# Kernel optimization log

Hardware: AMD Instinct MI355X
Metric: run time of the kernel (lower is better)

## Reference

```python
import jax, jax.numpy as jnp
import numpy as np

E = 1024
H = 16
HD = 64
LN_EPS = 1e-5


def _layernorm(x, g, b):
    mu = jnp.mean(x, axis=-1, keepdims=True)
    var = jnp.mean((x - mu) ** 2, axis=-1, keepdims=True)
    return (x - mu) * jax.lax.rsqrt(var + LN_EPS) * g + b


def _positional(L):
    # PositionalEncoding: stepper = 1/10000^(arange(0,E,2)/E); cat(sin, cos) -> [L, E]
    stepper = 1.0 / (10000.0 ** (jnp.arange(0, E, 2, dtype=jnp.float32) / E))
    args = jnp.arange(L, dtype=jnp.float32)[:, None] * stepper[None, :]  # [L, E/2]
    return jnp.concatenate([jnp.sin(args), jnp.cos(args)], axis=1)  # [L, E]


def setup_inputs() -> dict:
    key = jax.random.key(0)
    ks = jax.random.split(key, 8)
    s = 1.0 / np.sqrt(E)
    return {
        "sequences": jax.random.normal(ks[0], (4, 2048, E), dtype=jnp.float32),
        "W_q": jax.random.normal(ks[1], (E, E), dtype=jnp.float32) * s,
        "W_k": jax.random.normal(ks[2], (E, E), dtype=jnp.float32) * s,
        "W_v": jax.random.normal(ks[3], (E, E), dtype=jnp.float32) * s,
        "W_o": jax.random.normal(ks[4], (E, E), dtype=jnp.float32) * s,
        "ln1_g": jnp.ones((E,), jnp.float32),
        "ln1_b": jnp.zeros((E,), jnp.float32),
        "lin_W": jax.random.normal(ks[5], (E, E), dtype=jnp.float32) * s,  # torch Linear weight [out,in]
        "lin_b": jnp.zeros((E,), jnp.float32),
        "ln2_g": jnp.ones((E,), jnp.float32),
        "ln2_b": jnp.zeros((E,), jnp.float32),
    }


def reference(sequences, W_q, W_k, W_v, W_o, ln1_g, ln1_b, lin_W, lin_b, ln2_g, ln2_b):
    B, L, _ = sequences.shape
    x = sequences + _positional(L)[None]  # add positional embeddings
    # projections (no bias)
    q = (x @ W_q).reshape(B, L, H, HD).transpose(0, 2, 1, 3)  # [B,H,L,hd]
    k = (x @ W_k).reshape(B, L, H, HD).transpose(0, 2, 1, 3)
    v = (x @ W_v).reshape(B, L, H, HD).transpose(0, 2, 1, 3)
    # linear (softmax-free) attention: (Q K^T / sqrt(hd)) V
    scores = jnp.einsum("bhqd,bhkd->bhqk", q, k) / jnp.sqrt(jnp.float32(HD))
    ctx = jnp.einsum("bhqk,bhkd->bhqd", scores, v)
    ctx = ctx.transpose(0, 2, 1, 3).reshape(B, L, E)
    attn_out = ctx @ W_o
    h = _layernorm(x + attn_out, ln1_g, ln1_b)
    ff = jax.nn.relu(h @ lin_W.T + lin_b)
    return _layernorm(ff + h, ln2_g, ln2_b)
```

## Files before the change

kernel.cpp:

```cpp
#include <hip/hip_runtime.h>
#include <cstdint>

typedef unsigned short u16;
typedef __bf16 bf16x8 __attribute__((ext_vector_type(8)));
typedef float f32x4 __attribute__((ext_vector_type(4)));

__device__ __forceinline__ u16 f2bf(float f) {
    unsigned u = __float_as_uint(f);
    u += 0x7fffu + ((u >> 16) & 1u);
    return (u16)(u >> 16);
}
__device__ __forceinline__ float bf2f(u16 h) {
    return __uint_as_float(((unsigned)h) << 16);
}

__device__ __forceinline__ void lds16(const void* g, void* l) {
    __builtin_amdgcn_global_load_lds(
        (const __attribute__((address_space(1))) void*)g,
        (__attribute__((address_space(3))) void*)l, 16, 0, 0);
}

__global__ __launch_bounds__(256) void prep_x(const float* __restrict__ seq,
                                              float* __restrict__ x,
                                              u16* __restrict__ xb) {
    size_t i = (size_t)blockIdx.x * 256 + threadIdx.x;
    int e4 = (int)(i & 255) * 4;
    int l  = (int)((i >> 8) & 2047);
    float4 s = ((const float4*)seq)[i];
    float v[4] = {s.x, s.y, s.z, s.w};
    const float c = -13.287712379549449f / 512.0f;
#pragma unroll
    for (int j = 0; j < 4; j++) {
        int e  = e4 + j;
        int ii = e & 511;
        float st  = exp2f(c * (float)ii);
        float arg = (float)l * st;
        v[j] += (e < 512) ? sinf(arg) : cosf(arg);
    }
    float4 o; o.x = v[0]; o.y = v[1]; o.z = v[2]; o.w = v[3];
    ((float4*)x)[i] = o;
    ushort4 ob; ob.x = f2bf(v[0]); ob.y = f2bf(v[1]); ob.z = f2bf(v[2]); ob.w = f2bf(v[3]);
    ((ushort4*)xb)[i] = ob;
}

__global__ void prep_w(const float* __restrict__ wq, const float* __restrict__ wk,
                       const float* __restrict__ wv, const float* __restrict__ wo,
                       const float* __restrict__ wl, u16* __restrict__ wt) {
    int mat = blockIdx.z;
    const float* src = (mat == 0) ? wq : (mat == 1) ? wk : (mat == 2) ? wv : (mat == 3) ? wo : wl;
    u16* dst = wt + (size_t)mat * 1024 * 1024;
    int tx = threadIdx.x, ty = threadIdx.y;
    if (mat == 4) {
        int col = blockIdx.x * 32 + tx, row0 = blockIdx.y * 32;
#pragma unroll
        for (int j = 0; j < 32; j += 8)
            dst[(size_t)(row0 + ty + j) * 1024 + col] = f2bf(src[(size_t)(row0 + ty + j) * 1024 + col]);
    } else {
        __shared__ float tile[32][33];
        int col = blockIdx.x * 32 + tx, row0 = blockIdx.y * 32;
#pragma unroll
        for (int j = 0; j < 32; j += 8)
            tile[ty + j][tx] = src[(size_t)(row0 + ty + j) * 1024 + col];
        __syncthreads();
        int col2 = blockIdx.y * 32 + tx, row20 = blockIdx.x * 32;
#pragma unroll
        for (int j = 0; j < 32; j += 8)
            dst[(size_t)(row20 + ty + j) * 1024 + col2] = f2bf(tile[tx][ty + j]);
    }
}

template <int EPI>
__global__ __launch_bounds__(512) void gemm8p(const u16* __restrict__ A,
                                              const u16* __restrict__ Bt,
                                              void* __restrict__ Cv,
                                              const float* __restrict__ bias,
                                              int N, int K, int lda, size_t bstride) {
    __shared__ __align__(16) u16 lds[49152];
    const int t = threadIdx.x;
    const int ntn = N >> 8;
    const int nwg = gridDim.x;
    int bid = (int)blockIdx.x;
    bid = (bid & 7) * (nwg >> 3) + (bid >> 3);
    const int tm = bid / ntn, tn = bid - tm * ntn;
    const size_t m0 = (size_t)tm << 7, n0 = (size_t)tn << 8;
    const int w = t >> 6, lane = t & 63;
    const int wr = w >> 2, wc = w & 3;
    const u16* Bt_e = Bt + (bstride ? (m0 >> 11) * bstride : 0);

    const int r0 = t >> 3;
    const int ksrc = (t & 7) ^ (r0 & 7);
    const u16* sA0 = A + (m0 + r0) * (size_t)lda + ksrc * 8;
    const u16* sA1 = sA0 + (size_t)64 * lda;
    const u16* sB0 = Bt_e + (n0 + r0) * (size_t)K + ksrc * 8;
    const u16* sB1 = sB0 + (size_t)64 * K;
    const u16* sB2 = sB0 + (size_t)128 * K;
    const u16* sB3 = sB0 + (size_t)192 * K;
    u16* dstW = lds + (w << 9);

    const int ao = ((wr << 6) | (lane & 15)) << 6;
    const int bo = 8192 + ((((wc << 6) | (lane & 15))) << 6);
    const int kx = lane & 7;
    const int ks0 = (((lane >> 4) ^ kx) << 3);
    const int ks1 = (((4 + (lane >> 4)) ^ kx) << 3);

    f32x4 acc[4][4];
#pragma unroll
    for (int i = 0; i < 4; i++)
#pragma unroll
        for (int j = 0; j < 4; j++)
#pragma unroll
            for (int r = 0; r < 4; r++) acc[i][j][r] = 0.0f;

    const int NT = K >> 6;
    lds16(sA0, dstW);          lds16(sA1, dstW + 4096);
    lds16(sB0, dstW + 8192);   lds16(sB1, dstW + 12288);
    lds16(sB2, dstW + 16384);  lds16(sB3, dstW + 20480);

    for (int kt = 0; kt < NT; kt++) {
        const int b = kt & 1;
        asm volatile("" ::: "memory");
        if (kt + 1 < NT) {
            const size_t ko = (size_t)(kt + 1) << 6;
            u16* d = dstW + (b ^ 1) * 24576;
            lds16(sA0 + ko, d);          lds16(sA1 + ko, d + 4096);
            lds16(sB0 + ko, d + 8192);   lds16(sB1 + ko, d + 12288);
            lds16(sB2 + ko, d + 16384);  lds16(sB3 + ko, d + 20480);
            asm volatile("s_waitcnt vmcnt(6)" ::: "memory");
        } else {
            asm volatile("s_waitcnt vmcnt(0)" ::: "memory");
        }
        __builtin_amdgcn_s_barrier();
        asm volatile("" ::: "memory");
        const u16* Lb = lds + b * 24576;
#pragma unroll
        for (int kc = 0; kc < 2; kc++) {
            const int ksl = kc ? ks1 : ks0;
            bf16x8 af[4], bfr[4];
#pragma unroll
            for (int i = 0; i < 4; i++)
                af[i] = *reinterpret_cast<const bf16x8*>(Lb + ao + i * 1024 + ksl);
#pragma unroll
            for (int j = 0; j < 4; j++)
                bfr[j] = *reinterpret_cast<const bf16x8*>(Lb + bo + j * 1024 + ksl);
            __builtin_amdgcn_s_setprio(1);
#pragma unroll
            for (int i = 0; i < 4; i++)
#pragma unroll
                for (int j = 0; j < 4; j++)
                    acc[i][j] = __builtin_amdgcn_mfma_f32_16x16x32_bf16(af[i], bfr[j], acc[i][j], 0, 0, 0);
            __builtin_amdgcn_s_setprio(0);
        }
        asm volatile("" ::: "memory");
        __builtin_amdgcn_s_barrier();
    }

    const int crow = (lane >> 4) << 2, ccol = lane & 15;
#pragma unroll
    for (int i = 0; i < 4; i++)
#pragma unroll
        for (int j = 0; j < 4; j++) {
            size_t row = m0 + (wr << 6) + (i << 4) + crow;
            size_t col = n0 + (wc << 6) + (j << 4) + ccol;
#pragma unroll
            for (int r = 0; r < 4; r++) {
                float v = acc[i][j][r];
                if (EPI == 1) { v += bias[col]; v = fmaxf(v, 0.0f); }
                if (EPI == 2) ((u16*)Cv)[(row + r) * (size_t)N + col] = f2bf(v);
                else          ((float*)Cv)[(row + r) * (size_t)N + col] = v;
            }
        }
}

__global__ __launch_bounds__(256) void ktv_kernel(const u16* __restrict__ qkv,
                                                  float* __restrict__ part) {
    const int bh = blockIdx.x, split = blockIdx.y;
    const int b = bh >> 4, h = bh & 15;
    const u16* Kp = qkv + (size_t)b * 2048 * 3072 + 1024 + h * 64;
    const u16* Vp = Kp + 1024;
    __shared__ float ks[8][64], vs[8][64];
    float acc[16];
#pragma unroll
    for (int i = 0; i < 16; i++) acc[i] = 0.0f;
    const int t = threadIdx.x, r = t >> 4, c = t & 15;
    const int lr = t >> 5, lc = (t & 31) * 2;
    for (int l0 = split * 128; l0 < split * 128 + 128; l0 += 8) {
        unsigned kk = *(const unsigned*)(Kp + (size_t)(l0 + lr) * 3072 + lc);
        unsigned vv = *(const unsigned*)(Vp + (size_t)(l0 + lr) * 3072 + lc);
        ks[lr][lc] = bf2f((u16)kk); ks[lr][lc + 1] = bf2f((u16)(kk >> 16));
        vs[lr][lc] = bf2f((u16)vv); vs[lr][lc + 1] = bf2f((u16)(vv >> 16));
        __syncthreads();
#pragma unroll
        for (int i = 0; i < 8; i++) {
            float kv[4], vw[4];
#pragma unroll
            for (int a = 0; a < 4; a++) { kv[a] = ks[i][r + 16 * a]; vw[a] = vs[i][c + 16 * a]; }
#pragma unroll
            for (int a = 0; a < 4; a++)
#pragma unroll
                for (int q = 0; q < 4; q++) acc[a * 4 + q] += kv[a] * vw[q];
        }
        __syncthreads();
    }
    float* o = part + ((size_t)split * 64 + bh) * 4096;
#pragma unroll
    for (int a = 0; a < 4; a++)
#pragma unroll
        for (int q = 0; q < 4; q++) o[(r + 16 * a) * 64 + (c + 16 * q)] = acc[a * 4 + q];
}

__global__ __launch_bounds__(256) void ktv_reduce(const float* __restrict__ part,
                                                  float* __restrict__ ktv) {
    int i = blockIdx.x * 256 + threadIdx.x;
    float s = 0.0f;
#pragma unroll
    for (int sp = 0; sp < 16; sp++) s += part[(size_t)sp * 262144 + i];
    ktv[i] = s;
}

__global__ __launch_bounds__(256) void wprime_kernel(const float* __restrict__ ktv,
                                                     const float* __restrict__ Wo,
                                                     u16* __restrict__ wp) {
    const int n = blockIdx.x * 256 + threadIdx.x;
    const int h = blockIdx.y, b = blockIdx.z;
    const float* kt = ktv + ((size_t)(b * 16 + h) << 12);
    float acc[64];
#pragma unroll
    for (int i = 0; i < 64; i++) acc[i] = 0.0f;
    for (int j = 0; j < 64; j++) {
        float w = Wo[(size_t)(h * 64 + j) * 1024 + n];
#pragma unroll
        for (int i = 0; i < 64; i++) acc[i] += kt[i * 64 + j] * w;
    }
    u16* o = wp + ((size_t)b << 20) + (size_t)n * 1024 + h * 64;
    u16 ob[64];
#pragma unroll
    for (int i = 0; i < 64; i++) ob[i] = f2bf(acc[i] * 0.125f);
#pragma unroll
    for (int i = 0; i < 8; i++)
        ((uint4*)o)[i] = ((const uint4*)ob)[i];
}

__global__ __launch_bounds__(256) void ln_kernel(const float* __restrict__ A,
                                                 const float* __restrict__ B,
                                                 const float* __restrict__ g,
                                                 const float* __restrict__ be,
                                                 float* __restrict__ outF,
                                                 u16* __restrict__ outB) {
    __shared__ float sm[4];
    const int row = blockIdx.x, t = threadIdx.x;
    const float4 a = ((const float4*)(A + (size_t)row * 1024))[t];
    const float4 b = ((const float4*)(B + (size_t)row * 1024))[t];
    float x0 = a.x + b.x, x1 = a.y + b.y, x2 = a.z + b.z, x3 = a.w + b.w;
    float s = x0 + x1 + x2 + x3;
#pragma unroll
    for (int off = 32; off > 0; off >>= 1) s += __shfl_down(s, off);
    if ((t & 63) == 0) sm[t >> 6] = s;
    __syncthreads();
    const float mean = (sm[0] + sm[1] + sm[2] + sm[3]) * (1.0f / 1024.0f);
    __syncthreads();
    x0 -= mean; x1 -= mean; x2 -= mean; x3 -= mean;
    float s2 = x0 * x0 + x1 * x1 + x2 * x2 + x3 * x3;
#pragma unroll
    for (int off = 32; off > 0; off >>= 1) s2 += __shfl_down(s2, off);
    if ((t & 63) == 0) sm[t >> 6] = s2;
    __syncthreads();
    const float var = (sm[0] + sm[1] + sm[2] + sm[3]) * (1.0f / 1024.0f);
    const float rs = rsqrtf(var + 1e-5f);
    const float4 gv = ((const float4*)g)[t];
    const float4 bv = ((const float4*)be)[t];
    float y0 = x0 * rs * gv.x + bv.x;
    float y1 = x1 * rs * gv.y + bv.y;
    float y2 = x2 * rs * gv.z + bv.z;
    float y3 = x3 * rs * gv.w + bv.w;
    float4 o; o.x = y0; o.y = y1; o.z = y2; o.w = y3;
    ((float4*)(outF + (size_t)row * 1024))[t] = o;
    if (outB) {
        ushort4 ob; ob.x = f2bf(y0); ob.y = f2bf(y1); ob.z = f2bf(y2); ob.w = f2bf(y3);
        ((ushort4*)(outB + (size_t)row * 1024))[t] = ob;
    }
}

extern "C" void kernel_launch(void* const* d_in, const int* in_sizes, int n_in,
                              void* d_out, int out_size, void* d_ws, size_t ws_size,
                              hipStream_t stream) {
    const float* seq = (const float*)d_in[0];
    const float* Wq  = (const float*)d_in[1];
    const float* Wk  = (const float*)d_in[2];
    const float* Wv  = (const float*)d_in[3];
    const float* Wo  = (const float*)d_in[4];
    const float* g1  = (const float*)d_in[5];
    const float* b1  = (const float*)d_in[6];
    const float* Wl  = (const float*)d_in[7];
    const float* bl  = (const float*)d_in[8];
    const float* g2  = (const float*)d_in[9];
    const float* b2  = (const float*)d_in[10];

    char* ws = (char*)d_ws;
    const size_t MB = 1024 * 1024;
    float* x_f32 = (float*)(ws + 0);
    u16*   x_bf  = (u16*)(ws + 32 * MB);
    u16*   wt    = (u16*)(ws + 48 * MB);
    u16*   qkv   = (u16*)(ws + 58 * MB);
    float* ktv   = (float*)(ws + 106 * MB);
    float* attn  = (float*)(ws + 107 * MB);
    u16*   wpr   = (u16*)(ws + 139 * MB);
    float* kpart = (float*)(ws + 147 * MB);
    float* h1f   = (float*)(ws + 58 * MB);
    u16*   h1b   = (u16*)(ws + 90 * MB);
    float* ff    = (float*)(ws + 107 * MB);

    prep_x<<<dim3(8192), dim3(256), 0, stream>>>(seq, x_f32, x_bf);
    prep_w<<<dim3(32, 32, 5), dim3(32, 8), 0, stream>>>(Wq, Wk, Wv, Wo, Wl, wt);
    gemm8p<2><<<dim3(768), dim3(512), 0, stream>>>(x_bf, wt, qkv, nullptr,
                                                   3072, 1024, 1024, 0);
    ktv_kernel<<<dim3(64, 16), dim3(256), 0, stream>>>(qkv, kpart);
    ktv_reduce<<<dim3(1024), dim3(256), 0, stream>>>(kpart, ktv);
    wprime_kernel<<<dim3(4, 16, 4), dim3(256), 0, stream>>>(ktv, Wo, wpr);
    gemm8p<0><<<dim3(256), dim3(512), 0, stream>>>(qkv, wpr, attn, nullptr,
                                                   1024, 1024, 3072, (size_t)1024 * 1024);
    ln_kernel<<<dim3(8192), dim3(256), 0, stream>>>(x_f32, attn, g1, b1, h1f, h1b);
    gemm8p<1><<<dim3(256), dim3(512), 0, stream>>>(h1b, wt + (size_t)4 * 1024 * 1024, ff,
                                                   bl, 1024, 1024, 1024, 0);
    ln_kernel<<<dim3(8192), dim3(256), 0, stream>>>(ff, h1f, g2, b2, (float*)d_out, nullptr);
}
```

Measured before the change: 223.5 us.

## Fold W_q into per-batch attention weight, drop Q projection and fp32 x

Stops computing Q as a separate projection. Instead it multiplies W_q by the per-batch (K^T V)·W_o matrix to get a combined weight, then applies one GEMM from x. The QKV GEMM shrinks to KV only, and the fp32 copy of x is no longer stored because the positional term is recomputed inside the first layernorm. Attention and FFN outputs are written as bf16 to cut memory traffic, which adds rounding error and an extra small GEMM per batch.

Measured after the change: 212.6 us. 1.05x faster.

```diff
diff --git a/kernel.cpp b/kernel.cpp
--- a/kernel.cpp
+++ b/kernel.cpp
@@ -20,37 +20,35 @@
         (__attribute__((address_space(3))) void*)l, 16, 0, 0);
 }
 
+__device__ __forceinline__ float pos_term(int l, int e) {
+    const float c = -13.287712379549449f / 512.0f;
+    int ii = e & 511;
+    float st  = exp2f(c * (float)ii);
+    float arg = (float)l * st;
+    return (e < 512) ? sinf(arg) : cosf(arg);
+}
+
 __global__ __launch_bounds__(256) void prep_x(const float* __restrict__ seq,
-                                              float* __restrict__ x,
                                               u16* __restrict__ xb) {
     size_t i = (size_t)blockIdx.x * 256 + threadIdx.x;
     int e4 = (int)(i & 255) * 4;
     int l  = (int)((i >> 8) & 2047);
     float4 s = ((const float4*)seq)[i];
     float v[4] = {s.x, s.y, s.z, s.w};
-    const float c = -13.287712379549449f / 512.0f;
-#pragma unroll
-    for (int j = 0; j < 4; j++) {
-        int e  = e4 + j;
-        int ii = e & 511;
-        float st  = exp2f(c * (float)ii);
-        float arg = (float)l * st;
-        v[j] += (e < 512) ? sinf(arg) : cosf(arg);
-    }
-    float4 o; o.x = v[0]; o.y = v[1]; o.z = v[2]; o.w = v[3];
-    ((float4*)x)[i] = o;
+#pragma unroll
+    for (int j = 0; j < 4; j++) v[j] += pos_term(l, e4 + j);
     ushort4 ob; ob.x = f2bf(v[0]); ob.y = f2bf(v[1]); ob.z = f2bf(v[2]); ob.w = f2bf(v[3]);
     ((ushort4*)xb)[i] = ob;
 }
 
 __global__ void prep_w(const float* __restrict__ wq, const float* __restrict__ wk,
-                       const float* __restrict__ wv, const float* __restrict__ wo,
-                       const float* __restrict__ wl, u16* __restrict__ wt) {
+                       const float* __restrict__ wv, const float* __restrict__ wl,
+                       u16* __restrict__ wt) {
     int mat = blockIdx.z;
-    const float* src = (mat == 0) ? wq : (mat == 1) ? wk : (mat == 2) ? wv : (mat == 3) ? wo : wl;
+    const float* src = (mat == 0) ? wq : (mat == 1) ? wk : (mat == 2) ? wv : wl;
     u16* dst = wt + (size_t)mat * 1024 * 1024;
     int tx = threadIdx.x, ty = threadIdx.y;
-    if (mat == 4) {
+    if (mat == 0 || mat == 3) {
         int col = blockIdx.x * 32 + tx, row0 = blockIdx.y * 32;
 #pragma unroll
         for (int j = 0; j < 32; j += 8)
@@ -164,18 +162,18 @@
 #pragma unroll
             for (int r = 0; r < 4; r++) {
                 float v = acc[i][j][r];
-                if (EPI == 1) { v += bias[col]; v = fmaxf(v, 0.0f); }
-                if (EPI == 2) ((u16*)Cv)[(row + r) * (size_t)N + col] = f2bf(v);
-                else          ((float*)Cv)[(row + r) * (size_t)N + col] = v;
+                if (EPI == 3) { v += bias[col]; v = fmaxf(v, 0.0f); }
+                if (EPI == 0) ((float*)Cv)[(row + r) * (size_t)N + col] = v;
+                else          ((u16*)Cv)[(row + r) * (size_t)N + col] = f2bf(v);
             }
         }
 }
 
-__global__ __launch_bounds__(256) void ktv_kernel(const u16* __restrict__ qkv,
+__global__ __launch_bounds__(256) void ktv_kernel(const u16* __restrict__ kv,
                                                   float* __restrict__ part) {
     const int bh = blockIdx.x, split = blockIdx.y;
     const int b = bh >> 4, h = bh & 15;
-    const u16* Kp = qkv + (size_t)b * 2048 * 3072 + 1024 + h * 64;
+    const u16* Kp = kv + (size_t)b * 2048 * 2048 + h * 64;
     const u16* Vp = Kp + 1024;
     __shared__ float ks[8][64], vs[8][64];
     float acc[16];
@@ -184,20 +182,20 @@
     const int t = threadIdx.x, r = t >> 4, c = t & 15;
     const int lr = t >> 5, lc = (t & 31) * 2;
     for (int l0 = split * 128; l0 < split * 128 + 128; l0 += 8) {
-        unsigned kk = *(const unsigned*)(Kp + (size_t)(l0 + lr) * 3072 + lc);
-        unsigned vv = *(const unsigned*)(Vp + (size_t)(l0 + lr) * 3072 + lc);
+        unsigned kk = *(const unsigned*)(Kp + (size_t)(l0 + lr) * 2048 + lc);
+        unsigned vv = *(const unsigned*)(Vp + (size_t)(l0 + lr) * 2048 + lc);
         ks[lr][lc] = bf2f((u16)kk); ks[lr][lc + 1] = bf2f((u16)(kk >> 16));
         vs[lr][lc] = bf2f((u16)vv); vs[lr][lc + 1] = bf2f((u16)(vv >> 16));
         __syncthreads();
 #pragma unroll
         for (int i = 0; i < 8; i++) {
-            float kv[4], vw[4];
-#pragma unroll
-            for (int a = 0; a < 4; a++) { kv[a] = ks[i][r + 16 * a]; vw[a] = vs[i][c + 16 * a]; }
+            float kvr[4], vw[4];
+#pragma unroll
+            for (int a = 0; a < 4; a++) { kvr[a] = ks[i][r + 16 * a]; vw[a] = vs[i][c + 16 * a]; }
 #pragma unroll
             for (int a = 0; a < 4; a++)
 #pragma unroll
-                for (int q = 0; q < 4; q++) acc[a * 4 + q] += kv[a] * vw[q];
+                for (int q = 0; q < 4; q++) acc[a * 4 + q] += kvr[a] * vw[q];
         }
         __syncthreads();
     }
@@ -240,17 +238,21 @@
         ((uint4*)o)[i] = ((const uint4*)ob)[i];
 }
 
-__global__ __launch_bounds__(256) void ln_kernel(const float* __restrict__ A,
-                                                 const float* __restrict__ B,
-                                                 const float* __restrict__ g,
-                                                 const float* __restrict__ be,
-                                                 float* __restrict__ outF,
-                                                 u16* __restrict__ outB) {
+__global__ __launch_bounds__(256) void ln_pos(const float* __restrict__ seq,
+                                              const u16* __restrict__ attn,
+                                              const float* __restrict__ g,
+                                              const float* __restrict__ be,
+                                              float* __restrict__ outF,
+                                              u16* __restrict__ outB) {
     __shared__ float sm[4];
     const int row = blockIdx.x, t = threadIdx.x;
-    const float4 a = ((const float4*)(A + (size_t)row * 1024))[t];
-    const float4 b = ((const float4*)(B + (size_t)row * 1024))[t];
-    float x0 = a.x + b.x, x1 = a.y + b.y, x2 = a.z + b.z, x3 = a.w + b.w;
+    const int l = row & 2047, e4 = t * 4;
+    const float4 a = ((const float4*)(seq + (size_t)row * 1024))[t];
+    const ushort4 ab = ((const ushort4*)(attn + (size_t)row * 1024))[t];
+    float x0 = a.x + pos_term(l, e4 + 0) + bf2f(ab.x);
+    float x1 = a.y + pos_term(l, e4 + 1) + bf2f(ab.y);
+    float x2 = a.z + pos_term(l, e4 + 2) + bf2f(ab.z);
+    float x3 = a.w + pos_term(l, e4 + 3) + bf2f(ab.w);
     float s = x0 + x1 + x2 + x3;
 #pragma unroll
     for (int off = 32; off > 0; off >>= 1) s += __shfl_down(s, off);
@@ -274,10 +276,44 @@
     float y3 = x3 * rs * gv.w + bv.w;
     float4 o; o.x = y0; o.y = y1; o.z = y2; o.w = y3;
     ((float4*)(outF + (size_t)row * 1024))[t] = o;
-    if (outB) {
-        ushort4 ob; ob.x = f2bf(y0); ob.y = f2bf(y1); ob.z = f2bf(y2); ob.w = f2bf(y3);
-        ((ushort4*)(outB + (size_t)row * 1024))[t] = ob;
-    }
+    ushort4 ob; ob.x = f2bf(y0); ob.y = f2bf(y1); ob.z = f2bf(y2); ob.w = f2bf(y3);
+    ((ushort4*)(outB + (size_t)row * 1024))[t] = ob;
+}
+
+__global__ __launch_bounds__(256) void ln2_kernel(const u16* __restrict__ ff,
+                                                  const float* __restrict__ h1,
+                                                  const float* __restrict__ g,
+                                                  const float* __restrict__ be,
+                                                  float* __restrict__ outF) {
+    __shared__ float sm[4];
+    const int row = blockIdx.x, t = threadIdx.x;
+    const ushort4 fb = ((const ushort4*)(ff + (size_t)row * 1024))[t];
+    const float4 b = ((const float4*)(h1 + (size_t)row * 1024))[t];
+    float x0 = bf2f(fb.x) + b.x, x1 = bf2f(fb.y) + b.y;
+    float x2 = bf2f(fb.z) + b.z, x3 = bf2f(fb.w) + b.w;
+    float s = x0 + x1 + x2 + x3;
+#pragma unroll
+    for (int off = 32; off > 0; off >>= 1) s += __shfl_down(s, off);
+    if ((t & 63) == 0) sm[t >> 6] = s;
+    __syncthreads();
+    const float mean = (sm[0] + sm[1] + sm[2] + sm[3]) * (1.0f / 1024.0f);
+    __syncthreads();
+    x0 -= mean; x1 -= mean; x2 -= mean; x3 -= mean;
+    float s2 = x0 * x0 + x1 * x1 + x2 * x2 + x3 * x3;
+#pragma unroll
+    for (int off = 32; off > 0; off >>= 1) s2 += __shfl_down(s2, off);
+    if ((t & 63) == 0) sm[t >> 6] = s2;
+    __syncthreads();
+    const float var = (sm[0] + sm[1] + sm[2] + sm[3]) * (1.0f / 1024.0f);
+    const float rs = rsqrtf(var + 1e-5f);
+    const float4 gv = ((const float4*)g)[t];
+    const float4 bv = ((const float4*)be)[t];
+    float4 o;
+    o.x = x0 * rs * gv.x + bv.x;
+    o.y = x1 * rs * gv.y + bv.y;
+    o.z = x2 * rs * gv.z + bv.z;
+    o.w = x3 * rs * gv.w + bv.w;
+    ((float4*)(outF + (size_t)row * 1024))[t] = o;
 }
 
 extern "C" void kernel_launch(void* const* d_in, const int* in_sizes, int n_in,
@@ -297,29 +333,31 @@
 
     char* ws = (char*)d_ws;
     const size_t MB = 1024 * 1024;
-    float* x_f32 = (float*)(ws + 0);
-    u16*   x_bf  = (u16*)(ws + 32 * MB);
-    u16*   wt    = (u16*)(ws + 48 * MB);
-    u16*   qkv   = (u16*)(ws + 58 * MB);
-    float* ktv   = (float*)(ws + 106 * MB);
-    float* attn  = (float*)(ws + 107 * MB);
-    u16*   wpr   = (u16*)(ws + 139 * MB);
-    float* kpart = (float*)(ws + 147 * MB);
-    float* h1f   = (float*)(ws + 58 * MB);
-    u16*   h1b   = (u16*)(ws + 90 * MB);
-    float* ff    = (float*)(ws + 107 * MB);
-
-    prep_x<<<dim3(8192), dim3(256), 0, stream>>>(seq, x_f32, x_bf);
-    prep_w<<<dim3(32, 32, 5), dim3(32, 8), 0, stream>>>(Wq, Wk, Wv, Wo, Wl, wt);
-    gemm8p<2><<<dim3(768), dim3(512), 0, stream>>>(x_bf, wt, qkv, nullptr,
-                                                   3072, 1024, 1024, 0);
-    ktv_kernel<<<dim3(64, 16), dim3(256), 0, stream>>>(qkv, kpart);
+    u16*   x_bf  = (u16*)(ws + 0);
+    u16*   wt    = (u16*)(ws + 16 * MB);
+    u16*   kv    = (u16*)(ws + 24 * MB);
+    float* h1f   = (float*)(ws + 24 * MB);
+    float* kpart = (float*)(ws + 56 * MB);
+    u16*   attn  = (u16*)(ws + 56 * MB);
+    float* ktv   = (float*)(ws + 72 * MB);
+    u16*   wpr   = (u16*)(ws + 73 * MB);
+    u16*   wcomb = (u16*)(ws + 81 * MB);
+    u16*   h1b   = (u16*)(ws + 89 * MB);
+    u16*   ffb   = (u16*)(ws + 105 * MB);
+
+    prep_x<<<dim3(8192), dim3(256), 0, stream>>>(seq, x_bf);
+    prep_w<<<dim3(32, 32, 4), dim3(32, 8), 0, stream>>>(Wq, Wk, Wv, Wl, wt);
+    gemm8p<2><<<dim3(512), dim3(512), 0, stream>>>(x_bf, wt + (size_t)1 * MB, kv, nullptr,
+                                                   2048, 1024, 1024, 0);
+    ktv_kernel<<<dim3(64, 16), dim3(256), 0, stream>>>(kv, kpart);
     ktv_reduce<<<dim3(1024), dim3(256), 0, stream>>>(kpart, ktv);
     wprime_kernel<<<dim3(4, 16, 4), dim3(256), 0, stream>>>(ktv, Wo, wpr);
-    gemm8p<0><<<dim3(256), dim3(512), 0, stream>>>(qkv, wpr, attn, nullptr,
-                                                   1024, 1024, 3072, (size_t)1024 * 1024);
-    ln_kernel<<<dim3(8192), dim3(256), 0, stream>>>(x_f32, attn, g1, b1, h1f, h1b);
-    gemm8p<1><<<dim3(256), dim3(512), 0, stream>>>(h1b, wt + (size_t)4 * 1024 * 1024, ff,
+    gemm8p<2><<<dim3(128), dim3(512), 0, stream>>>(wpr, wt, wcomb, nullptr,
+                                                   1024, 1024, 1024, 0);
+    gemm8p<2><<<dim3(256), dim3(512), 0, stream>>>(x_bf, wcomb, attn, nullptr,
+                                                   1024, 1024, 1024, (size_t)1024 * 1024);
+    ln_pos<<<dim3(8192), dim3(256), 0, stream>>>(seq, attn, g1, b1, h1f, h1b);
+    gemm8p<3><<<dim3(256), dim3(512), 0, stream>>>(h1b, wt + (size_t)3 * MB, ffb,
                                                    bl, 1024, 1024, 1024, 0);
-    ln_kernel<<<dim3(8192), dim3(256), 0, stream>>>(ff, h1f, g2, b2, (float*)d_out, nullptr);
-}
+    ln2_kernel<<<dim3(8192), dim3(256), 0, stream>>>(ffb, h1f, g2, b2, (float*)d_out);
+}
```
